# Optimization experiments

Measured on AMD Instinct MI355X. Metric: run time of the kernel, lower is better.

The kernel has to match this reference:

```python
import jax, jax.numpy as jnp
import numpy as np

G, N0, E0 = 10000, 32, 64          # graphs, nodes/graph, edges/graph
NF, NEF, H, D = 64, 64, 128, 256   # num_features, num_edge_features, nhid, ddi_nhid
B = 4096                           # ddi batch_size (pos edges; neg edges follow)
NEG_DECAY = 0.5
RATIO = 0.5


def _lin(k, fan_in, shape):
    s = 1.0 / np.sqrt(fan_in)
    return jax.random.uniform(k, shape, jnp.float32, -s, s)


def setup_inputs() -> dict:
    key = jax.random.key(0)
    ks = jax.random.split(key, 40)
    N, E = G * N0, G * E0
    x = jax.random.normal(ks[0], (N, NF), jnp.float32)
    off = jnp.repeat(jnp.arange(G, dtype=jnp.int32) * N0, E0)
    edge_src = off + jax.random.randint(ks[1], (E,), 0, N0, jnp.int32)
    edge_dst = off + jax.random.randint(ks[2], (E,), 0, N0, jnp.int32)
    edge_weight = jax.random.uniform(ks[3], (E,), jnp.float32)
    ddi_edge_index = jax.random.randint(ks[4], (2, 2 * B), 0, G, jnp.int32)
    ddi_edge_attr = jax.random.normal(ks[5], (2 * B, NEF), jnp.float32)
    p = {}
    p['W1'] = _lin(ks[6], NF, (NF, H)); p['b1'] = jnp.zeros((H,), jnp.float32)
    p['Ws1r'] = _lin(ks[7], H, (H, 1)); p['Ws1n'] = _lin(ks[8], H, (H, 1)); p['bs1'] = jnp.zeros((1,), jnp.float32)
    p['W2'] = _lin(ks[9], H, (H, H)); p['b2'] = jnp.zeros((H,), jnp.float32)
    p['Ws2r'] = _lin(ks[10], H, (H, 1)); p['Ws2n'] = _lin(ks[11], H, (H, 1)); p['bs2'] = jnp.zeros((1,), jnp.float32)
    p['W3'] = _lin(ks[12], H, (H, H)); p['b3'] = jnp.zeros((H,), jnp.float32)
    p['Ws3r'] = _lin(ks[13], H, (H, 1)); p['Ws3n'] = _lin(ks[14], H, (H, 1)); p['bs3'] = jnp.zeros((1,), jnp.float32)
    p['Wd'] = _lin(ks[15], 6 * H, (6 * H, D)); p['bd'] = jnp.zeros((D,), jnp.float32)
    p['Wl1'] = _lin(ks[16], D, (D, D)); p['bl1'] = _lin(ks[17], D, (D,))
    p['Wl2'] = _lin(ks[18], D, (D, D)); p['bl2'] = _lin(ks[19], D, (D,))
    p['Wl3'] = _lin(ks[20], NEF, (NEF, D)); p['bl3'] = _lin(ks[21], NEF, (D,))
    return dict(x=x, edge_src=edge_src, edge_dst=edge_dst, edge_weight=edge_weight,
                ddi_edge_index=ddi_edge_index, ddi_edge_attr=ddi_edge_attr, **p)


def gcn(x, src, dst, ew, W, b):
    # PyG GCNConv: add self-loops (weight 1), symmetric normalization, sum-aggregate
    h = x @ W                                              # [N, out]
    deg = jnp.zeros(x.shape[0], x.dtype).at[dst].add(ew) + 1.0
    dis = jax.lax.rsqrt(deg)
    norm = dis[src] * ew * dis[dst]                        # [E]
    out = jnp.zeros_like(h).at[dst].add(norm[:, None] * h[src])
    out = out + (dis * dis)[:, None] * h                   # self-loop term
    return out + b


def sag_pool(x, src, dst, ew, Wr, Wn, bn, n_per_graph):
    # SAGPooling: score = tanh(GraphConv(x)); keep top ceil(ratio*n) nodes per graph
    N, Hd = x.shape
    g = N // n_per_graph
    agg = jnp.zeros((N, Hd), x.dtype).at[dst].add(ew[:, None] * x[src])
    score = jnp.tanh((agg @ Wn + bn + x @ Wr)[:, 0])       # [N]
    k = int(np.ceil(RATIO * n_per_graph))
    topv, topi = jax.lax.top_k(score.reshape(g, n_per_graph), k)   # [g, k]
    perm = (jnp.arange(g, dtype=jnp.int32)[:, None] * n_per_graph + topi.astype(jnp.int32)).reshape(-1)
    xk = x[perm] * topv.reshape(-1)[:, None]               # gate kept nodes by score
    old2new = jnp.full((N,), -1, jnp.int32).at[perm].set(jnp.arange(g * k, dtype=jnp.int32))
    ns, nd = old2new[src], old2new[dst]
    valid = (ns >= 0) & (nd >= 0)
    new_ew = jnp.where(valid, ew, 0.0)                     # zero-weight == filtered edge
    ns = jnp.where(valid, ns, 0)
    nd = jnp.where(valid, nd, 0)
    return xk, ns, nd, new_ew, k


def readout(x, k):
    # gmp || gap with contiguous, equal-size graphs
    xg = x.reshape(-1, k, x.shape[1])
    return jnp.concatenate([xg.max(axis=1), xg.mean(axis=1)], axis=1)


def reference(x, edge_src, edge_dst, edge_weight, ddi_edge_index, ddi_edge_attr,
              W1, b1, Ws1r, Ws1n, bs1, W2, b2, Ws2r, Ws2n, bs2,
              W3, b3, Ws3r, Ws3n, bs3, Wd, bd, Wl1, bl1, Wl2, bl2, Wl3, bl3):
    h = jax.nn.relu(gcn(x, edge_src, edge_dst, edge_weight, W1, b1))
    h, s, d, ew, k1 = sag_pool(h, edge_src, edge_dst, edge_weight, Ws1r, Ws1n, bs1, N0)
    x1 = readout(h, k1)
    h = jax.nn.relu(gcn(h, s, d, ew, W2, b2))
    h, s, d, ew, k2 = sag_pool(h, s, d, ew, Ws2r, Ws2n, bs2, k1)
    x2 = readout(h, k2)
    h = jax.nn.relu(gcn(h, s, d, ew, W3, b3))
    h, s, d, ew, k3 = sag_pool(h, s, d, ew, Ws3r, Ws3n, bs3, k2)
    x3 = readout(h, k3)
    feat = jnp.concatenate([x1, x2, x3], axis=1)           # [G, 6H] drug features
    # dropout_ratio=0.0 (eval): identity
    ds, dd = ddi_edge_index[0], ddi_edge_index[1]
    dew = jnp.ones(ds.shape, feat.dtype)
    z = jax.nn.relu(gcn(feat, ds, dd, dew, Wd, bd))        # [G, D]
    src_f, tgt_f = z[ds], z[dd]
    pos_x = jax.nn.sigmoid(src_f[:B] @ Wl1 + bl1)
    pos_y = jax.nn.sigmoid(tgt_f[:B] @ Wl2 + bl2)
    neg_x = jax.nn.sigmoid(src_f[B:] @ Wl1 + bl1)
    neg_y = jax.nn.sigmoid(tgt_f[B:] @ Wl2 + bl2)
    pos_a = jax.nn.sigmoid(ddi_edge_attr[:B] @ Wl3 + bl3)
    neg_a = jax.nn.sigmoid(ddi_edge_attr[B:] @ Wl3 + bl3)
    lp = pos_x + pos_a - pos_y
    ln = neg_x + neg_a - neg_y
    norm_pos = jnp.linalg.norm(lp, axis=1)
    norm_neg = jnp.linalg.norm(ln, axis=1)
    loss = 2.0 * D - norm_pos + NEG_DECAY * norm_neg
    return loss, norm_pos, norm_neg, pos_x
```

## Files before the change

### kernel.cpp

```cpp
#include <hip/hip_runtime.h>
#include <math.h>

#define GG   10000
#define NN0  32
#define EE0  64
#define NFF  64
#define HH   128
#define DD   256
#define BB   4096
#define E2B  8192
#define SIXH 768
#define APAD 36
#define XTS  36
#define BPS  40

typedef unsigned short u16;
typedef __attribute__((ext_vector_type(8))) short short8v;
typedef __attribute__((ext_vector_type(4))) short short4v;
typedef __attribute__((ext_vector_type(4))) float f32x4;
typedef _Float16 h8f __attribute__((ext_vector_type(8)));
typedef _Float16 h4f __attribute__((ext_vector_type(4)));

static __device__ __forceinline__ u16 f2bf(float x) {
  unsigned u = __float_as_uint(x);
  return (u16)((u + 0x7FFFu + ((u >> 16) & 1u)) >> 16);
}
static __device__ __forceinline__ float bf2f(u16 h) {
  return __uint_as_float(((unsigned)h) << 16);
}


template<int M, int P, int KK, int K, int KP, bool FIRST, bool LAST>
__device__ __forceinline__ void stage(
    const _Float16* __restrict__ WTh, const _Float16* __restrict__ WTl,
    const float* __restrict__ bg,
    const float* __restrict__ Wr, const float* __restrict__ Wn, const float* __restrict__ bs,
    _Float16* Xth, _Float16* Xtl, _Float16* ybh, _Float16* ybl,
    _Float16* Bph, _Float16* Bpl, float* s_A,
    float* s_dis, float* s_score, int* s_rank, int* s_inv,
    float* s_v1p, float* s_v2p,
    int& src_r, int& dst_r, float& ew_r,
    u16* __restrict__ featg, int t)
{
  constexpr int RT  = (M > 16) ? 2 : 1;
  constexpr int CTW = (RT == 2) ? 4 : 2;
  constexpr int KF  = K / 32;
  constexpr int NS  = (RT == 2) ? 2 : 4;
  const int l = t & 63, w = t >> 6;
  const int l15 = l & 15, kb = l >> 4;

  if (t < EE0)
    atomicAdd(&s_A[dst_r*APAD + src_r], ew_r);
  __syncthreads();

  if (t < M) {
    float deg = 1.f;
#pragma unroll
    for (int m0 = 0; m0 < M; m0 += 4) {
      const float4 a4 = *(const float4*)(s_A + t*APAD + m0);
      deg += a4.x + a4.y + a4.z + a4.w;
    }
    s_dis[t] = rsqrtf(deg);
  }
  __syncthreads();

  {
    constexpr int NE = (M*32 + 255) / 256;
#pragma unroll
    for (int n = 0; n < NE; ++n) {
      const int idx = n*256 + t;
      if (NE*256 == M*32 || idx < M*32) {
        const int r = idx >> 5, p = idx & 31;
        float c = 0.f;
        if (FIRST) {
          const float dr = s_dis[r];
          c = dr * s_A[r*APAD + p] * s_dis[p] + ((p == r) ? dr*dr : 0.f);
        } else if (p < P) {
          const int rk = s_rank[p];
          if (rk < M) {
            const float sc = s_score[p];
            const float dr = s_dis[r];
            c = dr * s_A[r*APAD + rk] * s_dis[rk] * sc
              + ((rk == r) ? dr*dr*sc : 0.f);
          }
        }
        const _Float16 h = (_Float16)c;
        Bph[r*BPS + p] = h;
        Bpl[r*BPS + p] = (_Float16)((c - (float)h) * 2048.f);
      }
    }
  }
  __syncthreads();

#pragma unroll
  for (int s = 0; s < 2; ++s) {
    const int it = (RT == 2) ? s : 0;
    const int jt = (RT == 2) ? w : (2*w + s);
    const h8f ah = *(const h8f*)(Bph + (it*16 + l15)*BPS + kb*8);
    const h8f al = *(const h8f*)(Bpl + (it*16 + l15)*BPS + kb*8);
    const int f = jt*16 + l15;
    h8f bh, bl;
    {
      const h4f x0 = *(const h4f*)(Xth + f*XTS + kb*8);
      const h4f x1 = *(const h4f*)(Xth + f*XTS + kb*8 + 4);
      const h4f y0 = *(const h4f*)(Xtl + f*XTS + kb*8);
      const h4f y1 = *(const h4f*)(Xtl + f*XTS + kb*8 + 4);
#pragma unroll
      for (int u = 0; u < 4; ++u) {
        bh[u] = x0[u]; bh[u+4] = x1[u];
        bl[u] = y0[u]; bl[u+4] = y1[u];
      }
    }
    f32x4 a0 = {0.f,0.f,0.f,0.f}, a1 = {0.f,0.f,0.f,0.f};
    a0 = __builtin_amdgcn_mfma_f32_16x16x32_f16(ah, bh, a0, 0, 0, 0);
    a1 = __builtin_amdgcn_mfma_f32_16x16x32_f16(ah, bl, a1, 0, 0, 0);
    a1 = __builtin_amdgcn_mfma_f32_16x16x32_f16(al, bh, a1, 0, 0, 0);
#pragma unroll
    for (int j = 0; j < 4; ++j) {
      const int r  = it*16 + kb*4 + j;
      const float v = fmaf(a1[j], (1.f/2048.f), a0[j]);
      const _Float16 h = (_Float16)v;
      ybh[r*KP + f] = h;
      ybl[r*KP + f] = (_Float16)((v - (float)h) * 2048.f);
    }
  }
  __syncthreads();

  {
    const int rt   = (RT == 2) ? (w >> 1) : 0;
    const int ct0  = (RT == 2) ? ((w & 1) * CTW) : (w * CTW);
    const int slot = (RT == 2) ? (w & 1) : w;

    h8f ah[KF], al[KF];
#pragma unroll
    for (int kf = 0; kf < KF; ++kf) {
      ah[kf] = *(const h8f*)(ybh + (rt*16 + l15)*KP + kf*32 + kb*8);
      al[kf] = *(const h8f*)(ybl + (rt*16 + l15)*KP + kf*32 + kb*8);
    }
    float p1[4] = {0.f,0.f,0.f,0.f}, p2[4] = {0.f,0.f,0.f,0.f};
#pragma unroll
    for (int ci = 0; ci < CTW; ++ci) {
      const int ct = ct0 + ci;
      const int col = ct*16 + l15;
      f32x4 a0 = {0.f,0.f,0.f,0.f}, a1 = {0.f,0.f,0.f,0.f};
#pragma unroll
      for (int kf = 0; kf < KF; ++kf) {
        const h8f bh = *(const h8f*)(WTh + (size_t)col*K + kf*32 + kb*8);
        const h8f bl = *(const h8f*)(WTl + (size_t)col*K + kf*32 + kb*8);
        a0 = __builtin_amdgcn_mfma_f32_16x16x32_f16(ah[kf], bh, a0, 0, 0, 0);
        a1 = __builtin_amdgcn_mfma_f32_16x16x32_f16(ah[kf], bl, a1, 0, 0, 0);
        a1 = __builtin_amdgcn_mfma_f32_16x16x32_f16(al[kf], bh, a1, 0, 0, 0);
      }
      const float bb = bg[col], wnc = Wn[col], wrc = Wr[col];
#pragma unroll
      for (int j = 0; j < 4; ++j) {
        const int row = rt*16 + kb*4 + j;
        const float o = fmaxf(fmaf(a1[j], (1.f/2048.f), a0[j]) + bb, 0.f);
        const _Float16 h = (_Float16)o;
        Xth[col*XTS + row] = h;
        Xtl[col*XTS + row] = (_Float16)((o - (float)h) * 2048.f);
        p1[j] = fmaf(o, wnc, p1[j]);
        p2[j] = fmaf(o, wrc, p2[j]);
      }
    }
#pragma unroll
    for (int j = 0; j < 4; ++j) {
#pragma unroll
      for (int off = 8; off >= 1; off >>= 1) {
        p1[j] += __shfl_xor(p1[j], off);
        p2[j] += __shfl_xor(p2[j], off);
      }
    }
    if (l15 == 0) {
#pragma unroll
      for (int j = 0; j < 4; ++j) {
        const int row = rt*16 + kb*4 + j;
        s_v1p[slot*32 + row] = p1[j];
        s_v2p[slot*32 + row] = p2[j];
      }
    }
  }
  __syncthreads();

  if (t < 64) {
    float v1t = 0.f, v2t = 0.f;
    if (t < M) {
      v2t = s_v2p[t] + s_v2p[32 + t];
      if (NS == 4) v2t += s_v2p[64 + t] + s_v2p[96 + t];
      float sc = bs[0] + v2t;
#pragma unroll
      for (int m0 = 0; m0 < M; m0 += 4) {
        const float4 a4 = *(const float4*)(s_A + t*APAD + m0);
        float4 v4 = *(const float4*)(s_v1p + m0);
        const float4 vb = *(const float4*)(s_v1p + 32 + m0);
        v4.x += vb.x; v4.y += vb.y; v4.z += vb.z; v4.w += vb.w;
        if (NS == 4) {
          const float4 vc = *(const float4*)(s_v1p + 64 + m0);
          const float4 vd = *(const float4*)(s_v1p + 96 + m0);
          v4.x += vc.x + vd.x; v4.y += vc.y + vd.y;
          v4.z += vc.z + vd.z; v4.w += vc.w + vd.w;
        }
        sc += a4.x*v4.x + a4.y*v4.y + a4.z*v4.z + a4.w*v4.w;
      }
      s_score[t] = tanhf(sc);
    }
    if (t < M) {
      const float st = s_score[t];
      int r = 0;
      for (int m = 0; m < M; ++m) {
        const float sm = s_score[m];
        r += (sm > st) || (sm == st && m < t);
      }
      s_rank[t] = r;
      if (r < KK) s_inv[r] = t;
    }
    if (!LAST) {
      const int a = s_rank[src_r];
      const int b = s_rank[dst_r];
      const bool val = (a < KK) && (b < KK);
      ew_r  = val ? ew_r : 0.f;
      src_r = val ? a : 0;
      dst_r = val ? b : 0;
    }
  }
  __syncthreads();

  {
    const int f = t & 127, which = t >> 7;
    float r_acc = which ? 0.f : -INFINITY;
#pragma unroll
    for (int r = 0; r < KK; ++r) {
      const int n = s_inv[r];
      const float v = (float)Xth[f*XTS + n] * s_score[n];
      r_acc = which ? (r_acc + v) : fmaxf(r_acc, v);
    }
    featg[which*HH + f] = f2bf(which ? r_acc * (1.f/KK) : r_acc);
  }
  if (!LAST) {
    for (int idx = t; idx < NN0*APAD/4; idx += 256) {
      float4 z4; z4.x = 0.f; z4.y = 0.f; z4.z = 0.f; z4.w = 0.f;
      *(float4*)(s_A + idx*4) = z4;
    }
  }
  __syncthreads();
}

__global__ __launch_bounds__(256, 4) void graph_kernel(
    const float* __restrict__ x,
    const int* __restrict__ esrc, const int* __restrict__ edst, const float* __restrict__ ewg,
    const _Float16* __restrict__ WT,
    const float* __restrict__ b1,
    const float* __restrict__ Ws1r, const float* __restrict__ Ws1n, const float* __restrict__ bs1,
    const float* __restrict__ b2,
    const float* __restrict__ Ws2r, const float* __restrict__ Ws2n, const float* __restrict__ bs2,
    const float* __restrict__ b3,
    const float* __restrict__ Ws3r, const float* __restrict__ Ws3n, const float* __restrict__ bs3,
    u16* __restrict__ featB)
{
  __shared__ __align__(16) _Float16 Xth[128*XTS], Xtl[128*XTS];
  __shared__ __align__(16) _Float16 ybh[2304], ybl[2304];
  __shared__ __align__(16) _Float16 Bph[32*BPS], Bpl[32*BPS];
  __shared__ __align__(16) float s_A[NN0*APAD];
  __shared__ __align__(16) float s_dis[NN0], s_score[NN0];
  __shared__ __align__(16) float s_v1p[128], s_v2p[128];
  __shared__ __align__(16) int   s_rank[NN0], s_inv[NN0];

  const int t = threadIdx.x;
  const int g = blockIdx.x;

#pragma unroll
  for (int q = 0; q < 8; ++q) {
    const int idx = q*256 + t;
    const int p = idx >> 6, f = idx & 63;
    const float v = x[(size_t)g*(NN0*NFF) + idx];
    const _Float16 h = (_Float16)v;
    Xth[f*XTS + p] = h;
    Xtl[f*XTS + p] = (_Float16)((v - (float)h) * 2048.f);
  }
  int src_r, dst_r; float ew_r;
  {
    const int e = g*EE0 + (t & 63);
    src_r = esrc[e] - g*NN0;
    dst_r = edst[e] - g*NN0;
    ew_r  = ewg[e];
  }
  for (int idx = t; idx < NN0*APAD/4; idx += 256) {
    float4 z4; z4.x = 0.f; z4.y = 0.f; z4.z = 0.f; z4.w = 0.f;
    *(float4*)(s_A + idx*4) = z4;
  }
  __syncthreads();

  u16* featg = featB + (size_t)g * SIXH;
  const _Float16* W1h = WT;
  const _Float16* W1l = W1h + 128*64;
  const _Float16* W2h = W1l + 128*64;
  const _Float16* W2l = W2h + 128*128;
  const _Float16* W3h = W2l + 128*128;
  const _Float16* W3l = W3h + 128*128;

  stage<32, 32, 16,  64,  72, true,  false>(W1h, W1l, b1, Ws1r, Ws1n, bs1,
      Xth, Xtl, ybh, ybl, Bph, Bpl, s_A, s_dis, s_score, s_rank, s_inv,
      s_v1p, s_v2p, src_r, dst_r, ew_r, featg, t);
  stage<16, 32,  8, 128, 136, false, false>(W2h, W2l, b2, Ws2r, Ws2n, bs2,
      Xth, Xtl, ybh, ybl, Bph, Bpl, s_A, s_dis, s_score, s_rank, s_inv,
      s_v1p, s_v2p, src_r, dst_r, ew_r, featg + 256, t);
  stage< 8, 16,  4, 128, 136, false, true >(W3h, W3l, b3, Ws3r, Ws3n, bs3,
      Xth, Xtl, ybh, ybl, Bph, Bpl, s_A, s_dis, s_score, s_rank, s_inv,
      s_v1p, s_v2p, src_r, dst_r, ew_r, featg + 512, t);
}

__global__ void k_convW123(const float* __restrict__ W1, const float* __restrict__ W2,
                           const float* __restrict__ W3, _Float16* __restrict__ T)
{
  const int c = blockIdx.x;
  const int k = threadIdx.x;
  _Float16* W1h = T;
  _Float16* W1l = W1h + 128*64;
  _Float16* W2h = W1l + 128*64;
  _Float16* W2l = W2h + 128*128;
  _Float16* W3h = W2l + 128*128;
  _Float16* W3l = W3h + 128*128;
  if (k < 64) {
    const float v = W1[(size_t)k*HH + c];
    const _Float16 h = (_Float16)v;
    W1h[c*64 + k] = h;
    W1l[c*64 + k] = (_Float16)((v - (float)h) * 2048.f);
  }
  {
    const float v = W2[(size_t)k*HH + c];
    const _Float16 h = (_Float16)v;
    W2h[c*HH + k] = h;
    W2l[c*HH + k] = (_Float16)((v - (float)h) * 2048.f);
  }
  {
    const float v = W3[(size_t)k*HH + c];
    const _Float16 h = (_Float16)v;
    W3h[c*HH + k] = h;
    W3l[c*HH + k] = (_Float16)((v - (float)h) * 2048.f);
  }
}


__global__ void k_convW(const float* __restrict__ Wd,
                        const float* __restrict__ Wl1, const float* __restrict__ Wl2,
                        u16* __restrict__ WdT, u16* __restrict__ WlT)
{
  const int b = blockIdx.x, t = threadIdx.x;
  if (b < 256) {
#pragma unroll
    for (int i = 0; i < 3; ++i) {
      const int k = i*256 + t;
      WdT[(size_t)b*SIXH + k] = f2bf(Wd[(size_t)k*DD + b]);
    }
  } else {
    const int c = b - 256;
    const float* src = (c < 256) ? Wl1 : Wl2;
    WlT[(size_t)c*DD + t] = f2bf(src[(size_t)t*DD + (c & 255)]);
  }
}

__global__ void k_deg_init(float* __restrict__ degf) {
  int i = blockIdx.x*256 + threadIdx.x;
  if (i < GG) degf[i] = 1.f;
}

__global__ void k_deg_acc(const int* __restrict__ ddi, float* __restrict__ degf) {
  int e = blockIdx.x*256 + threadIdx.x;
  if (e < E2B) atomicAdd(&degf[ddi[E2B + e]], 1.f);
}

__global__ __launch_bounds__(256) void k_ddi_mfma(const u16* __restrict__ featB,
    const u16* __restrict__ WdT, const float* __restrict__ degf,
    const float* __restrict__ bd, float* __restrict__ hdd, float* __restrict__ z)
{
  const int t = threadIdx.x;
  const int l = t & 63, w = t >> 6;
  const int r0 = blockIdx.x * 16;
  const int l15 = l & 15, kb = l >> 4;
  const int c0 = w * 64;
  f32x4 acc[4];
#pragma unroll
  for (int fi = 0; fi < 4; ++fi) { acc[fi][0]=0.f; acc[fi][1]=0.f; acc[fi][2]=0.f; acc[fi][3]=0.f; }
  const u16* aptr = featB + (size_t)(r0 + l15)*SIXH + kb*8;
#pragma unroll 2
  for (int kk = 0; kk < SIXH; kk += 32) {
    const short8v a = *(const short8v*)(aptr + kk);
#pragma unroll
    for (int fi = 0; fi < 4; ++fi) {
      const short8v b = *(const short8v*)(WdT + (size_t)(c0 + fi*16 + l15)*SIXH + kk + kb*8);
      acc[fi] = __builtin_amdgcn_mfma_f32_16x16x32_bf16(a, b, acc[fi], 0, 0, 0);
    }
  }
#pragma unroll
  for (int j = 0; j < 4; ++j) {
    const int gr = r0 + kb*4 + j;
    const float rd = 1.f / degf[gr];
#pragma unroll
    for (int fi = 0; fi < 4; ++fi) {
      const int c = c0 + fi*16 + l15;
      const float v = acc[fi][j];
      hdd[(size_t)gr*DD + c] = v;
      z[(size_t)gr*DD + c] = fmaf(v, rd, bd[c]);
    }
  }
}

__global__ void k_scatter(const int* __restrict__ ddi, const float* __restrict__ degf,
                          const float* __restrict__ hdd, float* __restrict__ z)
{
  const int t = threadIdx.x;
#pragma unroll
  for (int j = 0; j < 4; ++j) {
    const int e = blockIdx.x*4 + j;
    const int s = ddi[e], d = ddi[E2B + e];
    const float nrm = rsqrtf(degf[s]) * rsqrtf(degf[d]);
    atomicAdd(&z[(size_t)d*DD + t], nrm * hdd[(size_t)s*DD + t]);
  }
}

__global__ void k_zsplit(const float* __restrict__ z,
                         u16* __restrict__ zh, u16* __restrict__ zl)
{
  const int i4 = blockIdx.x*256 + threadIdx.x;
  const float4 v = *(const float4*)(z + (size_t)i4*4);
  short4v h, lo;
  {
    const u16 h0 = f2bf(v.x); h[0] = (short)h0; lo[0] = (short)f2bf(v.x - bf2f(h0));
    const u16 h1 = f2bf(v.y); h[1] = (short)h1; lo[1] = (short)f2bf(v.y - bf2f(h1));
    const u16 h2 = f2bf(v.z); h[2] = (short)h2; lo[2] = (short)f2bf(v.z - bf2f(h2));
    const u16 h3 = f2bf(v.w); h[3] = (short)h3; lo[3] = (short)f2bf(v.w - bf2f(h3));
  }
  *(short4v*)(zh + (size_t)i4*4) = h;
  *(short4v*)(zl + (size_t)i4*4) = lo;
}

__global__ __launch_bounds__(256) void k_xy_mfma(const u16* __restrict__ zh,
    const u16* __restrict__ zl, const u16* __restrict__ WlT,
    const float* __restrict__ bl1, const float* __restrict__ bl2,
    float* __restrict__ X, float* __restrict__ Y)
{
  const int t = threadIdx.x;
  const int l = t & 63, w = t >> 6;
  const int r0 = blockIdx.x * 16;
  const int l15 = l & 15, kb = l >> 4;
  const int c0 = w * 128;
  f32x4 acc[8];
#pragma unroll
  for (int fi = 0; fi < 8; ++fi) { acc[fi][0]=0.f; acc[fi][1]=0.f; acc[fi][2]=0.f; acc[fi][3]=0.f; }
  const u16* ah = zh + (size_t)(r0 + l15)*DD + kb*8;
  const u16* al = zl + (size_t)(r0 + l15)*DD + kb*8;
#pragma unroll 1
  for (int kk = 0; kk < DD; kk += 32) {
    const short8v a0 = *(const short8v*)(ah + kk);
    const short8v a1 = *(const short8v*)(al + kk);
#pragma unroll
    for (int fi = 0; fi < 8; ++fi) {
      const short8v b = *(const short8v*)(WlT + (size_t)(c0 + fi*16 + l15)*DD + kk + kb*8);
      acc[fi] = __builtin_amdgcn_mfma_f32_16x16x32_bf16(a0, b, acc[fi], 0, 0, 0);
      acc[fi] = __builtin_amdgcn_mfma_f32_16x16x32_bf16(a1, b, acc[fi], 0, 0, 0);
    }
  }
#pragma unroll
  for (int fi = 0; fi < 8; ++fi) {
    const int cg = c0 + fi*16 + l15;
    float* dst = (cg < 256) ? X : Y;
    const float bias = (cg < 256) ? bl1[cg] : bl2[cg - 256];
    const int c = cg & 255;
#pragma unroll
    for (int j = 0; j < 4; ++j) {
      const int gr = r0 + kb*4 + j;
      dst[(size_t)gr*DD + c] = 1.f / (1.f + expf(-(acc[fi][j] + bias)));
    }
  }
}

__global__ __launch_bounds__(256) void k_edge(const float* __restrict__ X,
    const float* __restrict__ Y, const int* __restrict__ ddi,
    const float* __restrict__ attr,
    const float* __restrict__ Wl3, const float* __restrict__ bl3,
    float* __restrict__ out)
{
  __shared__ __align__(16) float s_a[8*68];
  __shared__ __align__(16) float s_r[8*257];
  const int t = threadIdx.x;
  const int e0 = blockIdx.x * 8;
  for (int idx = t; idx < 8*64; idx += 256) {
    const int r = idx >> 6, k = idx & 63;
    s_a[r*68 + k] = attr[(size_t)(e0 + r)*NFF + k];
  }
  __syncthreads();
  float acc[8];
#pragma unroll
  for (int r = 0; r < 8; ++r) acc[r] = bl3[t];
#pragma unroll 4
  for (int k = 0; k < 64; ++k) {
    const float w = Wl3[(size_t)k*DD + t];
#pragma unroll
    for (int r = 0; r < 8; ++r) acc[r] = fmaf(s_a[r*68 + k], w, acc[r]);
  }
#pragma unroll
  for (int r = 0; r < 8; ++r) {
    const int e = e0 + r;
    const int s = ddi[e], d = ddi[E2B + e];
    const float xv = X[(size_t)s*DD + t];
    const float yv = Y[(size_t)d*DD + t];
    const float av = 1.f / (1.f + expf(-acc[r]));
    const float lp = xv + av - yv;
    s_r[r*257 + t] = lp * lp;
    if (e < BB) out[12288 + (size_t)e*DD + t] = xv;
  }
  __syncthreads();
  {
    const int row = t >> 5, l = t & 31;
    float s = 0.f;
#pragma unroll
    for (int j = 0; j < 8; ++j) s += s_r[row*257 + l + 32*j];
#pragma unroll
    for (int off = 16; off >= 1; off >>= 1) s += __shfl_xor(s, off);
    if (l == 0) {
      const float nrm = sqrtf(s);
      const int e = e0 + row;
      if (e < BB) out[4096 + e] = nrm;
      else        out[8192 + (e - BB)] = nrm;
    }
  }
}

__global__ void k_loss(float* __restrict__ out) {
  int i = blockIdx.x*256 + threadIdx.x;
  if (i < BB) out[i] = 2.f*(float)DD - out[4096 + i] + 0.5f*out[8192 + i];
}


extern "C" void kernel_launch(void* const* d_in, const int* in_sizes, int n_in,
                              void* d_out, int out_size, void* d_ws, size_t ws_size,
                              hipStream_t stream)
{
  const float* x    = (const float*)d_in[0];
  const int*   esrc = (const int*)d_in[1];
  const int*   edst = (const int*)d_in[2];
  const float* ewt  = (const float*)d_in[3];
  const int*   ddi  = (const int*)d_in[4];
  const float* attr = (const float*)d_in[5];
  const float* W1   = (const float*)d_in[6];  const float* b1  = (const float*)d_in[7];
  const float* Ws1r = (const float*)d_in[8];  const float* Ws1n= (const float*)d_in[9];  const float* bs1 = (const float*)d_in[10];
  const float* W2   = (const float*)d_in[11]; const float* b2  = (const float*)d_in[12];
  const float* Ws2r = (const float*)d_in[13]; const float* Ws2n= (const float*)d_in[14]; const float* bs2 = (const float*)d_in[15];
  const float* W3   = (const float*)d_in[16]; const float* b3  = (const float*)d_in[17];
  const float* Ws3r = (const float*)d_in[18]; const float* Ws3n= (const float*)d_in[19]; const float* bs3 = (const float*)d_in[20];
  const float* Wd   = (const float*)d_in[21]; const float* bd  = (const float*)d_in[22];
  const float* Wl1  = (const float*)d_in[23]; const float* bl1 = (const float*)d_in[24];
  const float* Wl2  = (const float*)d_in[25]; const float* bl2 = (const float*)d_in[26];
  const float* Wl3  = (const float*)d_in[27]; const float* bl3 = (const float*)d_in[28];

  float* ws = (float*)d_ws;
  u16*  featB = (u16*)ws;
  float* hdd  = ws + 3840000;
  float* zb   = hdd + (size_t)GG*DD;
  float* degf = zb  + (size_t)GG*DD;
  u16*  zh    = (u16*)(degf + GG);
  u16*  zl    = zh + (size_t)GG*DD;
  u16*  WdT   = zl + (size_t)GG*DD;
  u16*  WlT   = WdT + 256*SIXH;
  _Float16* WgT = (_Float16*)(WlT + 512*DD);
  float* Xb   = ws;
  float* Yb   = hdd;
  float* out  = (float*)d_out;

  k_convW<<<768, 256, 0, stream>>>(Wd, Wl1, Wl2, WdT, WlT);
  k_convW123<<<128, 128, 0, stream>>>(W1, W2, W3, WgT);
  graph_kernel<<<GG, 256, 0, stream>>>(x, esrc, edst, ewt, WgT,
      b1, Ws1r, Ws1n, bs1, b2, Ws2r, Ws2n, bs2, b3, Ws3r, Ws3n, bs3, featB);
  k_deg_init<<<(GG + 255)/256, 256, 0, stream>>>(degf);
  k_deg_acc<<<(E2B + 255)/256, 256, 0, stream>>>(ddi, degf);
  k_ddi_mfma<<<GG/16, 256, 0, stream>>>(featB, WdT, degf, bd, hdd, zb);
  k_scatter<<<E2B/4, 256, 0, stream>>>(ddi, degf, hdd, zb);
  k_zsplit<<<GG*DD/4/256, 256, 0, stream>>>(zb, zh, zl);
  k_xy_mfma<<<GG/16, 256, 0, stream>>>(zh, zl, WlT, bl1, bl2, Xb, Yb);
  k_edge<<<E2B/8, 256, 0, stream>>>(Xb, Yb, ddi, attr, Wl3, bl3, out);
  k_loss<<<(BB + 255)/256, 256, 0, stream>>>(out);
}
```

Before: 379.0 us.

## Restructure graph pooling stages to cut block barriers with double-buffered adjacency

Each stage's pooling and readout is reorganized so that the adjacency matrix for the next stage is built by a single wave (wave barriers plus shuffles) instead of through several block-wide __syncthreads. The adjacency is double-buffered, and the normalized propagation matrix is built in registers directly as MFMA operands rather than staged through shared memory. Each readout is deferred into the start of the next stage. The aim is to remove block-level synchronization and shared-memory round trips in the per-graph kernel. The cost is more per-lane recomputation, and the code now relies on wave-level ordering being correct for the single-wave sections.

```diff
diff --git a/kernel.cpp b/kernel.cpp
--- a/kernel.cpp
+++ b/kernel.cpp
@@ -12,7 +12,6 @@
 #define SIXH 768
 #define APAD 36
 #define XTS  36
-#define BPS  40
 
 typedef unsigned short u16;
 typedef __attribute__((ext_vector_type(8))) short short8v;
@@ -21,6 +20,8 @@
 typedef _Float16 h8f __attribute__((ext_vector_type(8)));
 typedef _Float16 h4f __attribute__((ext_vector_type(4)));
 
+#define WSYNC() do { __builtin_amdgcn_wave_barrier(); __builtin_amdgcn_sched_barrier(0); } while (0)
+
 static __device__ __forceinline__ u16 f2bf(float x) {
   unsigned u = __float_as_uint(x);
   return (u16)((u + 0x7FFFu + ((u >> 16) & 1u)) >> 16);
@@ -30,17 +31,17 @@
 }
 
 
-template<int M, int P, int KK, int K, int KP, bool FIRST, bool LAST>
+template<int M, int KK, int PREVKK, int K, int KP, bool LAST>
 __device__ __forceinline__ void stage(
     const _Float16* __restrict__ WTh, const _Float16* __restrict__ WTl,
     const float* __restrict__ bg,
     const float* __restrict__ Wr, const float* __restrict__ Wn, const float* __restrict__ bs,
     _Float16* Xth, _Float16* Xtl, _Float16* ybh, _Float16* ybl,
-    _Float16* Bph, _Float16* Bpl, float* s_A,
-    float* s_dis, float* s_score, int* s_rank, int* s_inv,
+    float* s_Acur, float* s_Anext,
+    float* s_dis, float* s_score, float* s_cm, int* s_rk, int* s_inv,
     float* s_v1p, float* s_v2p,
     int& src_r, int& dst_r, float& ew_r,
-    u16* __restrict__ featg, int t)
+    u16* __restrict__ featg_prev, int t)
 {
   constexpr int RT  = (M > 16) ? 2 : 1;
   constexpr int CTW = (RT == 2) ? 4 : 2;
@@ -49,55 +50,49 @@
   const int l = t & 63, w = t >> 6;
   const int l15 = l & 15, kb = l >> 4;
 
-  if (t < EE0)
-    atomicAdd(&s_A[dst_r*APAD + src_r], ew_r);
-  __syncthreads();
-
-  if (t < M) {
-    float deg = 1.f;
-#pragma unroll
-    for (int m0 = 0; m0 < M; m0 += 4) {
-      const float4 a4 = *(const float4*)(s_A + t*APAD + m0);
-      deg += a4.x + a4.y + a4.z + a4.w;
-    }
-    s_dis[t] = rsqrtf(deg);
-  }
-  __syncthreads();
-
-  {
-    constexpr int NE = (M*32 + 255) / 256;
-#pragma unroll
-    for (int n = 0; n < NE; ++n) {
-      const int idx = n*256 + t;
-      if (NE*256 == M*32 || idx < M*32) {
-        const int r = idx >> 5, p = idx & 31;
-        float c = 0.f;
-        if (FIRST) {
-          const float dr = s_dis[r];
-          c = dr * s_A[r*APAD + p] * s_dis[p] + ((p == r) ? dr*dr : 0.f);
-        } else if (p < P) {
-          const int rk = s_rank[p];
-          if (rk < M) {
-            const float sc = s_score[p];
-            const float dr = s_dis[r];
-            c = dr * s_A[r*APAD + rk] * s_dis[rk] * sc
-              + ((rk == r) ? dr*dr*sc : 0.f);
-          }
-        }
+  if constexpr (PREVKK > 0) {
+    const int f = t & 127, which = t >> 7;
+    float acc = which ? 0.f : -INFINITY;
+#pragma unroll
+    for (int r = 0; r < PREVKK; ++r) {
+      const int n = s_inv[r];
+      const float v = (float)Xth[f*XTS + n] * s_score[n];
+      acc = which ? (acc + v) : fmaxf(acc, v);
+    }
+    featg_prev[which*HH + f] = f2bf(which ? acc * (1.f/PREVKK) : acc);
+  }
+  if constexpr (!LAST) {
+    for (int idx = t; idx < NN0*APAD/4; idx += 256) {
+      float4 z4; z4.x=0.f; z4.y=0.f; z4.z=0.f; z4.w=0.f;
+      *(float4*)(s_Anext + idx*4) = z4;
+    }
+  }
+#pragma unroll
+  for (int s2 = 0; s2 < 2; ++s2) {
+    const int it = (RT == 2) ? s2 : 0;
+    const int jt = (RT == 2) ? w : (2*w + s2);
+    const int r  = it*16 + l15;
+    const float dr = s_dis[r];
+    h8f ah, al;
+    {
+      const int p0 = kb*8;
+      const int4   rkA = *(const int4*)(s_rk + p0);
+      const int4   rkB = *(const int4*)(s_rk + p0 + 4);
+      const float4 cmA = *(const float4*)(s_cm + p0);
+      const float4 cmB = *(const float4*)(s_cm + p0 + 4);
+#pragma unroll
+      for (int j = 0; j < 8; ++j) {
+        const int   rk = (j==0)?rkA.x:(j==1)?rkA.y:(j==2)?rkA.z:(j==3)?rkA.w
+                        :(j==4)?rkB.x:(j==5)?rkB.y:(j==6)?rkB.z:rkB.w;
+        const float cm = (j==0)?cmA.x:(j==1)?cmA.y:(j==2)?cmA.z:(j==3)?cmA.w
+                        :(j==4)?cmB.x:(j==5)?cmB.y:(j==6)?cmB.z:cmB.w;
+        const float a = s_Acur[r*APAD + rk];
+        const float c = dr * cm * (a + ((rk == r) ? 1.f : 0.f));
         const _Float16 h = (_Float16)c;
-        Bph[r*BPS + p] = h;
-        Bpl[r*BPS + p] = (_Float16)((c - (float)h) * 2048.f);
-      }
-    }
-  }
-  __syncthreads();
-
-#pragma unroll
-  for (int s = 0; s < 2; ++s) {
-    const int it = (RT == 2) ? s : 0;
-    const int jt = (RT == 2) ? w : (2*w + s);
-    const h8f ah = *(const h8f*)(Bph + (it*16 + l15)*BPS + kb*8);
-    const h8f al = *(const h8f*)(Bpl + (it*16 + l15)*BPS + kb*8);
+        ah[j] = h;
+        al[j] = (_Float16)((c - (float)h) * 2048.f);
+      }
+    }
     const int f = jt*16 + l15;
     h8f bh, bl;
     {
@@ -117,11 +112,11 @@
     a1 = __builtin_amdgcn_mfma_f32_16x16x32_f16(al, bh, a1, 0, 0, 0);
 #pragma unroll
     for (int j = 0; j < 4; ++j) {
-      const int r  = it*16 + kb*4 + j;
+      const int rr = it*16 + kb*4 + j;
       const float v = fmaf(a1[j], (1.f/2048.f), a0[j]);
       const _Float16 h = (_Float16)v;
-      ybh[r*KP + f] = h;
-      ybl[r*KP + f] = (_Float16)((v - (float)h) * 2048.f);
+      ybh[rr*KP + f] = h;
+      ybl[rr*KP + f] = (_Float16)((v - (float)h) * 2048.f);
     }
   }
   __syncthreads();
@@ -140,8 +135,7 @@
     float p1[4] = {0.f,0.f,0.f,0.f}, p2[4] = {0.f,0.f,0.f,0.f};
 #pragma unroll
     for (int ci = 0; ci < CTW; ++ci) {
-      const int ct = ct0 + ci;
-      const int col = ct*16 + l15;
+      const int col = (ct0 + ci)*16 + l15;
       f32x4 a0 = {0.f,0.f,0.f,0.f}, a1 = {0.f,0.f,0.f,0.f};
 #pragma unroll
       for (int kf = 0; kf < KF; ++kf) {
@@ -183,14 +177,15 @@
   __syncthreads();
 
   if (t < 64) {
-    float v1t = 0.f, v2t = 0.f;
+    float sc_own = 0.f;
+    int   rank   = 0;
     if (t < M) {
-      v2t = s_v2p[t] + s_v2p[32 + t];
+      float v2t = s_v2p[t] + s_v2p[32 + t];
       if (NS == 4) v2t += s_v2p[64 + t] + s_v2p[96 + t];
       float sc = bs[0] + v2t;
 #pragma unroll
       for (int m0 = 0; m0 < M; m0 += 4) {
-        const float4 a4 = *(const float4*)(s_A + t*APAD + m0);
+        const float4 a4 = *(const float4*)(s_Acur + t*APAD + m0);
         float4 v4 = *(const float4*)(s_v1p + m0);
         const float4 vb = *(const float4*)(s_v1p + 32 + m0);
         v4.x += vb.x; v4.y += vb.y; v4.z += vb.z; v4.w += vb.w;
@@ -202,44 +197,48 @@
         }
         sc += a4.x*v4.x + a4.y*v4.y + a4.z*v4.z + a4.w*v4.w;
       }
-      s_score[t] = tanhf(sc);
-    }
+      sc_own = tanhf(sc);
+      s_score[t] = sc_own;
+    }
+    WSYNC();
     if (t < M) {
-      const float st = s_score[t];
       int r = 0;
-      for (int m = 0; m < M; ++m) {
-        const float sm = s_score[m];
-        r += (sm > st) || (sm == st && m < t);
-      }
-      s_rank[t] = r;
+#pragma unroll
+      for (int m0 = 0; m0 < M; m0 += 4) {
+        const float4 s4 = *(const float4*)(s_score + m0);
+#pragma unroll
+        for (int q = 0; q < 4; ++q) {
+          const float sm = (q==0)?s4.x:(q==1)?s4.y:(q==2)?s4.z:s4.w;
+          r += (sm > sc_own) || (sm == sc_own && (m0+q) < t);
+        }
+      }
+      rank = r;
       if (r < KK) s_inv[r] = t;
     }
-    if (!LAST) {
-      const int a = s_rank[src_r];
-      const int b = s_rank[dst_r];
+    if constexpr (!LAST) {
+      const int a = __shfl(rank, src_r);
+      const int b = __shfl(rank, dst_r);
       const bool val = (a < KK) && (b < KK);
       ew_r  = val ? ew_r : 0.f;
       src_r = val ? a : 0;
       dst_r = val ? b : 0;
-    }
-  }
-  __syncthreads();
-
-  {
-    const int f = t & 127, which = t >> 7;
-    float r_acc = which ? 0.f : -INFINITY;
-#pragma unroll
-    for (int r = 0; r < KK; ++r) {
-      const int n = s_inv[r];
-      const float v = (float)Xth[f*XTS + n] * s_score[n];
-      r_acc = which ? (r_acc + v) : fmaxf(r_acc, v);
-    }
-    featg[which*HH + f] = f2bf(which ? r_acc * (1.f/KK) : r_acc);
-  }
-  if (!LAST) {
-    for (int idx = t; idx < NN0*APAD/4; idx += 256) {
-      float4 z4; z4.x = 0.f; z4.y = 0.f; z4.z = 0.f; z4.w = 0.f;
-      *(float4*)(s_A + idx*4) = z4;
+      atomicAdd(&s_Anext[dst_r*APAD + src_r], ew_r);
+      WSYNC();
+      if (t < 16) {
+        float deg = 1.f;
+#pragma unroll
+        for (int m0 = 0; m0 < 32; m0 += 4) {
+          const float4 a4 = *(const float4*)(s_Anext + t*APAD + m0);
+          deg += a4.x + a4.y + a4.z + a4.w;
+        }
+        s_dis[t] = rsqrtf(deg);
+      }
+      WSYNC();
+      if (t < 32) {
+        const bool valid = (t < M) && (rank < KK);
+        s_rk[t] = valid ? rank : 0;
+        s_cm[t] = valid ? s_dis[rank] * sc_own : 0.f;
+      }
     }
   }
   __syncthreads();
@@ -259,11 +258,10 @@
 {
   __shared__ __align__(16) _Float16 Xth[128*XTS], Xtl[128*XTS];
   __shared__ __align__(16) _Float16 ybh[2304], ybl[2304];
-  __shared__ __align__(16) _Float16 Bph[32*BPS], Bpl[32*BPS];
-  __shared__ __align__(16) float s_A[NN0*APAD];
-  __shared__ __align__(16) float s_dis[NN0], s_score[NN0];
+  __shared__ __align__(16) float s_A[2][NN0*APAD];
   __shared__ __align__(16) float s_v1p[128], s_v2p[128];
-  __shared__ __align__(16) int   s_rank[NN0], s_inv[NN0];
+  __shared__ __align__(16) float s_dis[NN0], s_score[NN0], s_cm[NN0];
+  __shared__ __align__(16) int   s_rk[NN0], s_inv[16];
 
   const int t = threadIdx.x;
   const int g = blockIdx.x;
@@ -285,8 +283,26 @@
     ew_r  = ewg[e];
   }
   for (int idx = t; idx < NN0*APAD/4; idx += 256) {
-    float4 z4; z4.x = 0.f; z4.y = 0.f; z4.z = 0.f; z4.w = 0.f;
-    *(float4*)(s_A + idx*4) = z4;
+    float4 z4; z4.x=0.f; z4.y=0.f; z4.z=0.f; z4.w=0.f;
+    *(float4*)(s_A[0] + idx*4) = z4;
+  }
+  __syncthreads();
+
+  if (t < 64) {
+    atomicAdd(&s_A[0][dst_r*APAD + src_r], ew_r);
+    WSYNC();
+    if (t < 32) {
+      float deg = 1.f;
+#pragma unroll
+      for (int m0 = 0; m0 < 32; m0 += 4) {
+        const float4 a4 = *(const float4*)(s_A[0] + t*APAD + m0);
+        deg += a4.x + a4.y + a4.z + a4.w;
+      }
+      const float dis = rsqrtf(deg);
+      s_dis[t] = dis;
+      s_cm[t]  = dis;
+      s_rk[t]  = t;
+    }
   }
   __syncthreads();
 
@@ -298,15 +314,27 @@
   const _Float16* W3h = W2l + 128*128;
   const _Float16* W3l = W3h + 128*128;
 
-  stage<32, 32, 16,  64,  72, true,  false>(W1h, W1l, b1, Ws1r, Ws1n, bs1,
-      Xth, Xtl, ybh, ybl, Bph, Bpl, s_A, s_dis, s_score, s_rank, s_inv,
+  stage<32, 16, 0,  64,  72, false>(W1h, W1l, b1, Ws1r, Ws1n, bs1,
+      Xth, Xtl, ybh, ybl, s_A[0], s_A[1], s_dis, s_score, s_cm, s_rk, s_inv,
       s_v1p, s_v2p, src_r, dst_r, ew_r, featg, t);
-  stage<16, 32,  8, 128, 136, false, false>(W2h, W2l, b2, Ws2r, Ws2n, bs2,
-      Xth, Xtl, ybh, ybl, Bph, Bpl, s_A, s_dis, s_score, s_rank, s_inv,
+  stage<16,  8, 16, 128, 136, false>(W2h, W2l, b2, Ws2r, Ws2n, bs2,
+      Xth, Xtl, ybh, ybl, s_A[1], s_A[0], s_dis, s_score, s_cm, s_rk, s_inv,
+      s_v1p, s_v2p, src_r, dst_r, ew_r, featg, t);
+  stage< 8,  4,  8, 128, 136, true >(W3h, W3l, b3, Ws3r, Ws3n, bs3,
+      Xth, Xtl, ybh, ybl, s_A[0], s_A[1], s_dis, s_score, s_cm, s_rk, s_inv,
       s_v1p, s_v2p, src_r, dst_r, ew_r, featg + 256, t);
-  stage< 8, 16,  4, 128, 136, false, true >(W3h, W3l, b3, Ws3r, Ws3n, bs3,
-      Xth, Xtl, ybh, ybl, Bph, Bpl, s_A, s_dis, s_score, s_rank, s_inv,
-      s_v1p, s_v2p, src_r, dst_r, ew_r, featg + 512, t);
+
+  {
+    const int f = t & 127, which = t >> 7;
+    float acc = which ? 0.f : -INFINITY;
+#pragma unroll
+    for (int r = 0; r < 4; ++r) {
+      const int n = s_inv[r];
+      const float v = (float)Xth[f*XTS + n] * s_score[n];
+      acc = which ? (acc + v) : fmaxf(acc, v);
+    }
+    featg[512 + which*HH + f] = f2bf(which ? acc * 0.25f : acc);
+  }
 }
 
 __global__ void k_convW123(const float* __restrict__ W1, const float* __restrict__ W2,
```

After: 387.0 us. 1.02x slower.
